# Kernel optimization log

Hardware: AMD Instinct MI355X
Metric: run time of the kernel (lower is better)

Reference implementation:

```python
import jax, jax.numpy as jnp
import numpy as np

GROUPS = 32
HEADS = 8
EPS = 1e-5

def setup_inputs() -> dict:
    key = jax.random.key(0)
    ks = jax.random.split(key, 5)
    C = 512
    x = jax.random.normal(ks[0], (8, C, 32, 32), dtype=jnp.float32)
    gn_w = jnp.ones((C,), dtype=jnp.float32)
    gn_b = jnp.zeros((C,), dtype=jnp.float32)
    qkv_w = jax.random.normal(ks[1], (3 * C, C), dtype=jnp.float32) * 0.02
    qkv_b = jnp.zeros((3 * C,), dtype=jnp.float32)
    proj_w = jax.random.normal(ks[2], (C, C), dtype=jnp.float32) * 0.02
    proj_b = jnp.zeros((C,), dtype=jnp.float32)
    return {"x": x, "gn_w": gn_w, "gn_b": gn_b, "qkv_w": qkv_w,
            "qkv_b": qkv_b, "proj_w": proj_w, "proj_b": proj_b}

def reference(x, gn_w, gn_b, qkv_w, qkv_b, proj_w, proj_b):
    B, C, H, W = x.shape
    d = C // HEADS
    # GroupNorm(32, C)
    xg = x.reshape(B, GROUPS, C // GROUPS, H, W)
    mean = xg.mean(axis=(2, 3, 4), keepdims=True)
    var = xg.var(axis=(2, 3, 4), keepdims=True)
    h = ((xg - mean) * jax.lax.rsqrt(var + EPS)).reshape(B, C, H, W)
    h = h * gn_w[None, :, None, None] + gn_b[None, :, None, None]
    # 1x1 conv QKV == channel matmul
    qkv = jnp.einsum('bchw,oc->bohw', h, qkv_w) + qkv_b[None, :, None, None]
    qkv = qkv.reshape(B, 3, HEADS, d, H * W)
    q, k, v = qkv[:, 0], qkv[:, 1], qkv[:, 2]  # [B, heads, d, HW]
    scale = d ** (-0.5)
    # weight[b,h,q,k] = sum_d q[b,h,d,q] * k[b,h,d,k] * scale
    attn = jax.nn.softmax(jnp.einsum('bhdq,bhdk->bhqk', q, k) * scale, axis=-1)
    # out[b,h,d,q] = sum_k v[b,h,d,k] * attn[b,h,q,k]
    out = jnp.einsum('bhdk,bhqk->bhdq', v, attn).reshape(B, C, H, W)
    out = jnp.einsum('bchw,oc->bohw', out, proj_w) + proj_b[None, :, None, None]
    return out + x
```

## Files before the change

### kernel.cpp

```cpp
#include <hip/hip_runtime.h>
#include <math.h>

#define B_    8
#define C_    512
#define HW_   1024
#define O3_   1536
#define HEADS_ 8
#define D_    64
#define G_    32
#define CPG_  16
#define EPS_  1e-5f
#define M_TOT 8192

#define QSCALE (0.125f * 1.44269504088896f)

typedef __bf16 bf16x8 __attribute__((ext_vector_type(8)));
typedef __bf16 bf16x4 __attribute__((ext_vector_type(4)));
typedef float  f32x4  __attribute__((ext_vector_type(4)));

__device__ __forceinline__ void async_copy16(void* lds, const void* g) {
  __builtin_amdgcn_global_load_lds(
      (const __attribute__((address_space(1))) unsigned int*)g,
      (__attribute__((address_space(3))) unsigned int*)lds, 16, 0, 0);
}

__global__ __launch_bounds__(1024) void k_gn(const float* __restrict__ x,
                                             const float* __restrict__ gw,
                                             const float* __restrict__ gb,
                                             __bf16* __restrict__ h,
                                             const float* __restrict__ qw,
                                             const float* __restrict__ pw,
                                             __bf16* __restrict__ qwb,
                                             __bf16* __restrict__ pwb) {
  __shared__ float red[34];
  __shared__ __bf16 T[16 * 1032];
  int tid = threadIdx.x;
  if (blockIdx.x >= B_ * G_) {
    int i0 = (blockIdx.x - B_ * G_) * 1024 + tid;
    for (int i = i0; i < O3_ * C_ / 4; i += 64 * 1024) {
      float4 v = ((const float4*)qw)[i];
      bf16x4 o = {(__bf16)v.x, (__bf16)v.y, (__bf16)v.z, (__bf16)v.w};
      ((bf16x4*)qwb)[i] = o;
    }
    for (int i = i0; i < C_ * C_ / 4; i += 64 * 1024) {
      float4 v = ((const float4*)pw)[i];
      bf16x4 o = {(__bf16)v.x, (__bf16)v.y, (__bf16)v.z, (__bf16)v.w};
      ((bf16x4*)pwb)[i] = o;
    }
    return;
  }
  int bg = blockIdx.x;
  int b = bg >> 5, g = bg & 31;
  const float4* xg4 = (const float4*)(x + ((size_t)(b * C_) + g * CPG_) * HW_);

  float s = 0.f, ss = 0.f;
  for (int i = tid; i < CPG_ * HW_ / 4; i += 1024) {
    float4 v = xg4[i];
    s += v.x + v.y + v.z + v.w;
    ss += v.x * v.x + v.y * v.y + v.z * v.z + v.w * v.w;
  }
  for (int off = 32; off > 0; off >>= 1) {
    s  += __shfl_down(s, off, 64);
    ss += __shfl_down(ss, off, 64);
  }
  int wv = tid >> 6;
  if ((tid & 63) == 0) { red[wv] = s; red[16 + wv] = ss; }
  __syncthreads();
  if (tid == 0) {
    float S = 0.f, SS = 0.f;
#pragma unroll
    for (int i = 0; i < 16; i++) { S += red[i]; SS += red[16 + i]; }
    float mean = S / (float)(CPG_ * HW_);
    float var  = SS / (float)(CPG_ * HW_) - mean * mean;
    red[32] = mean;
    red[33] = rsqrtf(var + EPS_);
  }
  __syncthreads();
  float mean = red[32], rstd = red[33];

  for (int i = tid; i < CPG_ * HW_ / 4; i += 1024) {
    int c = i >> 8;
    int hw4 = (i & 255) * 4;
    float ga = gw[g * CPG_ + c], be = gb[g * CPG_ + c];
    float4 v = xg4[i];
    bf16x4 pk;
    pk[0] = (__bf16)((v.x - mean) * rstd * ga + be);
    pk[1] = (__bf16)((v.y - mean) * rstd * ga + be);
    pk[2] = (__bf16)((v.z - mean) * rstd * ga + be);
    pk[3] = (__bf16)((v.w - mean) * rstd * ga + be);
    *(bf16x4*)(&T[c * 1032 + hw4]) = pk;
  }
  __syncthreads();

  __bf16* hb = h + (size_t)b * HW_ * C_ + g * CPG_;
  for (int j = tid; j < 2 * HW_; j += 1024) {
    int hw = j >> 1, c8 = (j & 1) * 8;
    bf16x8 v;
#pragma unroll
    for (int jj = 0; jj < 8; jj++) v[jj] = T[(c8 + jj) * 1032 + hw];
    *(bf16x8*)(hb + (size_t)hw * C_ + c8) = v;
  }
}

#define BKQ 32
__global__ __launch_bounds__(256, 3) void k_qkv(const __bf16* __restrict__ h,
                                                const __bf16* __restrict__ w,
                                                const float* __restrict__ bias,
                                                __bf16* __restrict__ y,
                                                __bf16* __restrict__ vT) {
  __shared__ __align__(16) __bf16 As[2][128 * BKQ];
  __shared__ __align__(16) __bf16 Bs[2][128 * BKQ];
  int m0 = blockIdx.x * 128, n0 = blockIdx.y * 128;
  int t = threadIdx.x;
  int lane = t & 63, l16 = lane & 15, quad = lane >> 4;
  int wv = t >> 6;
  int wm = (wv >> 1) * 64, wn = (wv & 1) * 64;

  int rsub = lane >> 2;
  int chunk = (lane & 3) ^ (rsub & 3);
  const __bf16* ag = h + (size_t)(m0 + wv * 32 + rsub) * C_ + chunk * 8;
  const __bf16* bg = w + (size_t)(n0 + wv * 32 + rsub) * C_ + chunk * 8;
  int sw = l16 & 3;

  auto stage = [&](int k0, int bi) {
    __bf16* la = As[bi] + wv * 1024 + lane * 8;
    __bf16* lb = Bs[bi] + wv * 1024 + lane * 8;
#pragma unroll
    for (int s = 0; s < 2; s++) {
      async_copy16(la + s * 512, ag + (size_t)(s * 16) * C_ + k0);
      async_copy16(lb + s * 512, bg + (size_t)(s * 16) * C_ + k0);
    }
  };

  f32x4 acc[4][4];
#pragma unroll
  for (int i = 0; i < 4; i++)
#pragma unroll
    for (int j = 0; j < 4; j++) acc[i][j] = f32x4{0.f, 0.f, 0.f, 0.f};

  stage(0, 0);
  stage(1 * BKQ, 1);
  for (int kk = 0; kk < 16; kk++) {
    int bi = kk & 1;
    if (kk < 15)
      asm volatile("s_waitcnt vmcnt(4)\n\ts_barrier" ::: "memory");
    else
      asm volatile("s_waitcnt vmcnt(0)\n\ts_barrier" ::: "memory");
    const __bf16* as = As[bi];
    const __bf16* bs = Bs[bi];
    bf16x8 af[4], bf[4];
#pragma unroll
    for (int i = 0; i < 4; i++) {
      af[i] = *(const bf16x8*)(as + (wm + i * 16 + l16) * BKQ + (quad ^ sw) * 8);
      bf[i] = *(const bf16x8*)(bs + (wn + i * 16 + l16) * BKQ + (quad ^ sw) * 8);
    }
    asm volatile("s_waitcnt lgkmcnt(0)\n\ts_barrier" ::: "memory");
    if (kk < 14) stage((kk + 2) * BKQ, bi);
    __builtin_amdgcn_s_setprio(1);
#pragma unroll
    for (int i = 0; i < 4; i++)
#pragma unroll
      for (int j = 0; j < 4; j++)
        acc[i][j] = __builtin_amdgcn_mfma_f32_16x16x32_bf16(af[i], bf[j],
                                                            acc[i][j], 0, 0, 0);
    __builtin_amdgcn_s_setprio(0);
  }

  if (n0 >= 2 * C_) {
    int bb = m0 >> 10;
    int tokBase = (m0 & 1023) + wm + quad * 4;
#pragma unroll
    for (int j = 0; j < 4; j++) {
      int n = n0 + wn + j * 16 + l16;
      int c = n - 2 * C_;
      float bv = bias[n];
      __bf16* vrow = vT + ((size_t)(bb * C_) + c) * HW_;
#pragma unroll
      for (int i = 0; i < 4; i++) {
        bf16x4 pk;
#pragma unroll
        for (int r = 0; r < 4; r++) pk[r] = (__bf16)(acc[i][j][r] + bv);
        *(bf16x4*)(vrow + tokBase + i * 16) = pk;
      }
    }
  } else {
    float sc = (n0 < C_) ? QSCALE : 1.0f;
#pragma unroll
    for (int j = 0; j < 4; j++) {
      int n = n0 + wn + j * 16 + l16;
      float bv = bias[n];
#pragma unroll
      for (int i = 0; i < 4; i++)
#pragma unroll
        for (int r = 0; r < 4; r++) {
          int m = m0 + wm + i * 16 + quad * 4 + r;
          y[(size_t)m * O3_ + n] = (__bf16)((acc[i][j][r] + bv) * sc);
        }
    }
  }
}

__global__ __launch_bounds__(256, 4) void k_attn(const __bf16* __restrict__ y,
                                                 const __bf16* __restrict__ vT,
                                                 __bf16* __restrict__ ao) {
  __shared__ __align__(16) __bf16 Ks[2][64 * 64];
  __shared__ __align__(16) __bf16 Vt[2][64 * 64];
  __shared__ __align__(16) __bf16 Pp[4][16 * 36];
  int hd = blockIdx.x, b = blockIdx.y, qt = blockIdx.z;
  int t = threadIdx.x;
  int wv = t >> 6, lane = t & 63, l16 = lane & 15, quad = lane >> 4;
  int q0 = qt * 64 + wv * 16;

  const __bf16* base = y + (size_t)(b * HW_) * O3_ + hd * D_;
  const __bf16* kg = base + C_;
  const __bf16* vtg = vT + ((size_t)(b * C_) + hd * D_) * HW_;

  bf16x8 qb[2];
#pragma unroll
  for (int dh = 0; dh < 2; dh++)
    qb[dh] = *(const bf16x8*)(base + (size_t)(q0 + l16) * O3_ +
                              dh * 32 + quad * 8);

  int rowsub = lane >> 3;
  int kChunk = (lane & 7) ^ (rowsub & 7);

  auto stage = [&](int kt, int bi) {
#pragma unroll
    for (int s = 0; s < 2; s++) {
      int row = wv * 16 + s * 8 + rowsub;
      async_copy16(&Ks[bi][(wv * 16 + s * 8) * 64 + lane * 8],
                   kg + (size_t)(kt + row) * O3_ + kChunk * 8);
    }
#pragma unroll
    for (int s = 0; s < 2; s++) {
      int row = wv * 16 + s * 8 + rowsub;
      async_copy16(&Vt[bi][(wv * 16 + s * 8) * 64 + lane * 8],
                   vtg + (size_t)row * HW_ + kt + kChunk * 8);
    }
  };

  float l_run = 0.f;
  f32x4 o_acc[4];
#pragma unroll
  for (int dt = 0; dt < 4; dt++) o_acc[dt] = f32x4{0.f, 0.f, 0.f, 0.f};

  f32x4 sE[2], sO[2];

  auto QK = [&](f32x4 (&st)[2], const __bf16* ks, int kh) {
    __builtin_amdgcn_s_setprio(1);
#pragma unroll
    for (int tti = 0; tti < 2; tti++) {
      int row = kh * 32 + tti * 16 + l16;
      bf16x8 ka0 = *(const bf16x8*)(&ks[row * 64 + ((quad) ^ (l16 & 7)) * 8]);
      bf16x8 ka1 = *(const bf16x8*)(&ks[row * 64 + ((4 + quad) ^ (l16 & 7)) * 8]);
      f32x4 z = {0.f, 0.f, 0.f, 0.f};
      st[tti] = __builtin_amdgcn_mfma_f32_16x16x32_bf16(ka0, qb[0], z, 0, 0, 0);
      st[tti] = __builtin_amdgcn_mfma_f32_16x16x32_bf16(ka1, qb[1], st[tti], 0, 0, 0);
    }
    __builtin_amdgcn_s_setprio(0);
  };

  auto FIN = [&](f32x4 (&st)[2], const __bf16* vs, int kh) {
    float rs = 0.f;
#pragma unroll
    for (int tti = 0; tti < 2; tti++)
#pragma unroll
      for (int r = 0; r < 4; r++) {
        float e = __builtin_amdgcn_exp2f(st[tti][r]);
        st[tti][r] = e;
        rs += e;
      }
    l_run += rs;
#pragma unroll
    for (int tti = 0; tti < 2; tti++) {
      bf16x4 pk;
#pragma unroll
      for (int r = 0; r < 4; r++) pk[r] = (__bf16)st[tti][r];
      *(bf16x4*)(&Pp[wv][l16 * 36 + tti * 16 + quad * 4]) = pk;
    }
    asm volatile("s_waitcnt lgkmcnt(0)" ::: "memory");
    bf16x8 pb = *(const bf16x8*)(&Pp[wv][l16 * 36 + quad * 8]);
    __builtin_amdgcn_s_setprio(1);
#pragma unroll
    for (int dt = 0; dt < 4; dt++) {
      bf16x8 va = *(const bf16x8*)(&vs[(dt * 16 + l16) * 64 +
                                       ((kh * 4 + quad) ^ (l16 & 7)) * 8]);
      o_acc[dt] = __builtin_amdgcn_mfma_f32_16x16x32_bf16(va, pb,
                                                          o_acc[dt], 0, 0, 0);
    }
    __builtin_amdgcn_s_setprio(0);
  };

  stage(0, 0);

  for (int step = 0; step < 16; step++) {
    int bi = step & 1;
    asm volatile("s_waitcnt vmcnt(0)\n\ts_barrier" ::: "memory");
    if (step < 15) stage((step + 1) * 64, bi ^ 1);

    const __bf16* ks = Ks[bi];
    const __bf16* vs = Vt[bi];
    QK(sE, ks, 0);
    QK(sO, ks, 1); FIN(sE, vs, 0);
    FIN(sO, vs, 1);
  }

  l_run += __shfl_xor(l_run, 16, 64);
  l_run += __shfl_xor(l_run, 32, 64);
  float inv = 1.f / l_run;

#pragma unroll
  for (int dt = 0; dt < 4; dt++) {
    bf16x4 pk;
#pragma unroll
    for (int r = 0; r < 4; r++) pk[r] = (__bf16)(o_acc[dt][r] * inv);
    int ch = hd * D_ + dt * 16 + quad * 4;
    *(bf16x4*)(ao + (size_t)(b * HW_ + q0 + l16) * C_ + ch) = pk;
  }
}

#define BK 64
__global__ __launch_bounds__(256) void k_proj(const __bf16* __restrict__ ao,
                                              const __bf16* __restrict__ w,
                                              const float* __restrict__ bias,
                                              const float* __restrict__ x,
                                              float* __restrict__ out) {
  __shared__ __align__(16) __bf16 As[2][128 * BK];
  __shared__ __align__(16) __bf16 Bs[2][64 * BK];
  int n0 = blockIdx.x * 64, m0 = blockIdx.y * 128;
  int t = threadIdx.x;
  int lane = t & 63, l16 = lane & 15, quad = lane >> 4;
  int wv = t >> 6;
  int wm = (wv >> 1) * 64, wn = (wv & 1) * 32;

  int rsub = lane >> 3;
  int chunk = (lane & 7) ^ rsub;
  const __bf16* ag = w + (size_t)(m0 + wv * 32 + rsub) * C_ + chunk * 8;
  const __bf16* bg = ao + (size_t)(n0 + wv * 16 + rsub) * C_ + chunk * 8;
  int sw = l16 & 7;

  auto stage = [&](int k0, int bi) {
    __bf16* la = As[bi] + wv * 2048 + lane * 8;
    __bf16* lb = Bs[bi] + wv * 1024 + lane * 8;
#pragma unroll
    for (int s = 0; s < 4; s++)
      async_copy16(la + s * 512, ag + (size_t)(s * 8) * C_ + k0);
#pragma unroll
    for (int s = 0; s < 2; s++)
      async_copy16(lb + s * 512, bg + (size_t)(s * 8) * C_ + k0);
  };

  f32x4 acc[4][2];
#pragma unroll
  for (int i = 0; i < 4; i++)
#pragma unroll
    for (int j = 0; j < 2; j++) acc[i][j] = f32x4{0.f, 0.f, 0.f, 0.f};

  stage(0, 0);
  stage(1 * BK, 1);
  for (int kk = 0; kk < 8; kk++) {
    int bi = kk & 1;
    if (kk < 7)
      asm volatile("s_waitcnt vmcnt(6)\n\ts_barrier" ::: "memory");
    else
      asm volatile("s_waitcnt vmcnt(0)\n\ts_barrier" ::: "memory");
    const __bf16* as = As[bi];
    const __bf16* bs = Bs[bi];
    bf16x8 af[2][4], bf[2][2];
#pragma unroll
    for (int hh = 0; hh < 2; hh++) {
#pragma unroll
      for (int i = 0; i < 4; i++)
        af[hh][i] = *(const bf16x8*)(as + (wm + i * 16 + l16) * BK +
                                     ((hh * 4 + quad) ^ sw) * 8);
#pragma unroll
      for (int j = 0; j < 2; j++)
        bf[hh][j] = *(const bf16x8*)(bs + (wn + j * 16 + l16) * BK +
                                     ((hh * 4 + quad) ^ sw) * 8);
    }
    asm volatile("s_waitcnt lgkmcnt(0)\n\ts_barrier" ::: "memory");
    if (kk < 6) stage((kk + 2) * BK, bi);
    __builtin_amdgcn_s_setprio(1);
#pragma unroll
    for (int hh = 0; hh < 2; hh++)
#pragma unroll
      for (int i = 0; i < 4; i++)
#pragma unroll
        for (int j = 0; j < 2; j++)
          acc[i][j] = __builtin_amdgcn_mfma_f32_16x16x32_bf16(af[hh][i], bf[hh][j],
                                                              acc[i][j], 0, 0, 0);
    __builtin_amdgcn_s_setprio(0);
  }

  int bb = n0 >> 10;
#pragma unroll
  for (int i = 0; i < 4; i++)
#pragma unroll
    for (int r = 0; r < 4; r++) {
      int o = m0 + wm + i * 16 + quad * 4 + r;
      float bv = bias[o];
#pragma unroll
      for (int j = 0; j < 2; j++) {
        int n = n0 + wn + j * 16 + l16;
        int hw = n & 1023;
        size_t idx = ((size_t)(bb * C_ + o)) * HW_ + hw;
        out[idx] = acc[i][j][r] + bv + x[idx];
      }
    }
}

extern "C" void kernel_launch(void* const* d_in, const int* in_sizes, int n_in,
                              void* d_out, int out_size, void* d_ws, size_t ws_size,
                              hipStream_t stream) {
  const float* x      = (const float*)d_in[0];
  const float* gn_w   = (const float*)d_in[1];
  const float* gn_b   = (const float*)d_in[2];
  const float* qkv_w  = (const float*)d_in[3];
  const float* qkv_b  = (const float*)d_in[4];
  const float* proj_w = (const float*)d_in[5];
  const float* proj_b = (const float*)d_in[6];
  float* out = (float*)d_out;

  char* ws = (char*)d_ws;
  __bf16* h   = (__bf16*)(ws);
  __bf16* qwb = (__bf16*)(ws + 8388608);
  __bf16* pwb = (__bf16*)(ws + 8388608 + 1572864);
  __bf16* yq  = (__bf16*)(ws + 8388608 + 1572864 + 524288);
  __bf16* ao  = (__bf16*)(ws + 8388608 + 1572864 + 524288 + 25165824);
  __bf16* vT  = (__bf16*)(ws + 8388608 + 1572864 + 524288 + 25165824 + 8388608);

  k_gn  <<<B_ * G_ + 64, 1024, 0, stream>>>(x, gn_w, gn_b, h,
                                            qkv_w, proj_w, qwb, pwb);
  k_qkv <<<dim3(M_TOT / 128, O3_ / 128, 1), 256, 0, stream>>>(h, qwb, qkv_b, yq, vT);
  k_attn<<<dim3(HEADS_, B_, 16), 256, 0, stream>>>(yq, vT, ao);
  k_proj<<<dim3(M_TOT / 64, C_ / 128, 1), 256, 0, stream>>>(ao, pwb, proj_b, x, out);
  (void)in_sizes; (void)n_in; (void)out_size; (void)ws_size;
}
```

Baseline: 142.7 us.

## Load V fragments directly from global into registers and double K tile size

The attention kernel no longer stages V through LDS. Each wave prefetches its V MFMA operands straight from global memory into registers one sub-tile ahead, while the K tile per step grows to 128 keys, halving the barrier count. The QKV GEMM changes its LDS swizzle and swaps MFMA operand order for Q/K outputs, so each lane holds four consecutive columns and can write packed bf16x4 stores with vector bias loads instead of scalar stores. The risk is more register pressure and uncoalesced, redundant global V reads across waves, since every wave loads the full V slice itself.

```diff
diff --git a/kernel.cpp b/kernel.cpp
--- a/kernel.cpp
+++ b/kernel.cpp
@@ -115,12 +115,13 @@
   int lane = t & 63, l16 = lane & 15, quad = lane >> 4;
   int wv = t >> 6;
   int wm = (wv >> 1) * 64, wn = (wv & 1) * 64;
+  bool vreg = (n0 >= 2 * C_);
 
   int rsub = lane >> 2;
-  int chunk = (lane & 3) ^ (rsub & 3);
+  int chunk = (lane & 3) ^ ((rsub >> 1) & 3);
   const __bf16* ag = h + (size_t)(m0 + wv * 32 + rsub) * C_ + chunk * 8;
   const __bf16* bg = w + (size_t)(n0 + wv * 32 + rsub) * C_ + chunk * 8;
-  int sw = l16 & 3;
+  int sw = (l16 >> 1) & 3;
 
   auto stage = [&](int k0, int bi) {
     __bf16* la = As[bi] + wv * 1024 + lane * 8;
@@ -157,16 +158,25 @@
     asm volatile("s_waitcnt lgkmcnt(0)\n\ts_barrier" ::: "memory");
     if (kk < 14) stage((kk + 2) * BKQ, bi);
     __builtin_amdgcn_s_setprio(1);
-#pragma unroll
-    for (int i = 0; i < 4; i++)
-#pragma unroll
-      for (int j = 0; j < 4; j++)
-        acc[i][j] = __builtin_amdgcn_mfma_f32_16x16x32_bf16(af[i], bf[j],
-                                                            acc[i][j], 0, 0, 0);
+    if (vreg) {
+#pragma unroll
+      for (int i = 0; i < 4; i++)
+#pragma unroll
+        for (int j = 0; j < 4; j++)
+          acc[i][j] = __builtin_amdgcn_mfma_f32_16x16x32_bf16(af[i], bf[j],
+                                                              acc[i][j], 0, 0, 0);
+    } else {
+#pragma unroll
+      for (int i = 0; i < 4; i++)
+#pragma unroll
+        for (int j = 0; j < 4; j++)
+          acc[i][j] = __builtin_amdgcn_mfma_f32_16x16x32_bf16(bf[j], af[i],
+                                                              acc[i][j], 0, 0, 0);
+    }
     __builtin_amdgcn_s_setprio(0);
   }
 
-  if (n0 >= 2 * C_) {
+  if (vreg) {
     int bb = m0 >> 10;
     int tokBase = (m0 & 1023) + wm + quad * 4;
 #pragma unroll
@@ -187,15 +197,18 @@
     float sc = (n0 < C_) ? QSCALE : 1.0f;
 #pragma unroll
     for (int j = 0; j < 4; j++) {
-      int n = n0 + wn + j * 16 + l16;
-      float bv = bias[n];
-#pragma unroll
-      for (int i = 0; i < 4; i++)
-#pragma unroll
-        for (int r = 0; r < 4; r++) {
-          int m = m0 + wm + i * 16 + quad * 4 + r;
-          y[(size_t)m * O3_ + n] = (__bf16)((acc[i][j][r] + bv) * sc);
-        }
+      int nb = n0 + wn + j * 16 + quad * 4;
+      float4 bv4 = *(const float4*)(bias + nb);
+      float bvs[4] = {bv4.x, bv4.y, bv4.z, bv4.w};
+#pragma unroll
+      for (int i = 0; i < 4; i++) {
+        int m = m0 + wm + i * 16 + l16;
+        bf16x4 pk;
+#pragma unroll
+        for (int r = 0; r < 4; r++)
+          pk[r] = (__bf16)((acc[i][j][r] + bvs[r]) * sc);
+        *(bf16x4*)(y + (size_t)m * O3_ + nb) = pk;
+      }
     }
   }
 }
@@ -203,8 +216,7 @@
 __global__ __launch_bounds__(256, 4) void k_attn(const __bf16* __restrict__ y,
                                                  const __bf16* __restrict__ vT,
                                                  __bf16* __restrict__ ao) {
-  __shared__ __align__(16) __bf16 Ks[2][64 * 64];
-  __shared__ __align__(16) __bf16 Vt[2][64 * 64];
+  __shared__ __align__(16) __bf16 Ks[2][128 * 64];
   __shared__ __align__(16) __bf16 Pp[4][16 * 36];
   int hd = blockIdx.x, b = blockIdx.y, qt = blockIdx.z;
   int t = threadIdx.x;
@@ -214,6 +226,7 @@
   const __bf16* base = y + (size_t)(b * HW_) * O3_ + hd * D_;
   const __bf16* kg = base + C_;
   const __bf16* vtg = vT + ((size_t)(b * C_) + hd * D_) * HW_;
+  const __bf16* vfb = vtg + (size_t)l16 * HW_ + quad * 8;
 
   bf16x8 qb[2];
 #pragma unroll
@@ -221,21 +234,15 @@
     qb[dh] = *(const bf16x8*)(base + (size_t)(q0 + l16) * O3_ +
                               dh * 32 + quad * 8);
 
-  int rowsub = lane >> 3;
-  int kChunk = (lane & 7) ^ (rowsub & 7);
+  int kRowSub = lane >> 3;
+  int kChunk = (lane & 7) ^ (kRowSub & 7);
 
   auto stage = [&](int kt, int bi) {
 #pragma unroll
-    for (int s = 0; s < 2; s++) {
-      int row = wv * 16 + s * 8 + rowsub;
-      async_copy16(&Ks[bi][(wv * 16 + s * 8) * 64 + lane * 8],
+    for (int s = 0; s < 4; s++) {
+      int row = wv * 32 + s * 8 + kRowSub;
+      async_copy16(&Ks[bi][(wv * 32 + s * 8) * 64 + lane * 8],
                    kg + (size_t)(kt + row) * O3_ + kChunk * 8);
-    }
-#pragma unroll
-    for (int s = 0; s < 2; s++) {
-      int row = wv * 16 + s * 8 + rowsub;
-      async_copy16(&Vt[bi][(wv * 16 + s * 8) * 64 + lane * 8],
-                   vtg + (size_t)row * HW_ + kt + kChunk * 8);
     }
   };
 
@@ -245,12 +252,19 @@
   for (int dt = 0; dt < 4; dt++) o_acc[dt] = f32x4{0.f, 0.f, 0.f, 0.f};
 
   f32x4 sE[2], sO[2];
+  bf16x8 vaE[4], vaO[4];
+
+  auto PFV = [&](bf16x8 (&va)[4], int off) {
+#pragma unroll
+    for (int dt = 0; dt < 4; dt++)
+      va[dt] = *(const bf16x8*)(vfb + (size_t)(dt * 16) * HW_ + off);
+  };
 
   auto QK = [&](f32x4 (&st)[2], const __bf16* ks, int kh) {
     __builtin_amdgcn_s_setprio(1);
 #pragma unroll
     for (int tti = 0; tti < 2; tti++) {
-      int row = kh * 32 + tti * 16 + l16;
+      int row = (kh * 2 + tti) * 16 + l16;
       bf16x8 ka0 = *(const bf16x8*)(&ks[row * 64 + ((quad) ^ (l16 & 7)) * 8]);
       bf16x8 ka1 = *(const bf16x8*)(&ks[row * 64 + ((4 + quad) ^ (l16 & 7)) * 8]);
       f32x4 z = {0.f, 0.f, 0.f, 0.f};
@@ -260,7 +274,7 @@
     __builtin_amdgcn_s_setprio(0);
   };
 
-  auto FIN = [&](f32x4 (&st)[2], const __bf16* vs, int kh) {
+  auto FIN = [&](f32x4 (&st)[2], bf16x8 (&va)[4]) {
     float rs = 0.f;
 #pragma unroll
     for (int tti = 0; tti < 2; tti++)
@@ -282,27 +296,27 @@
     bf16x8 pb = *(const bf16x8*)(&Pp[wv][l16 * 36 + quad * 8]);
     __builtin_amdgcn_s_setprio(1);
 #pragma unroll
-    for (int dt = 0; dt < 4; dt++) {
-      bf16x8 va = *(const bf16x8*)(&vs[(dt * 16 + l16) * 64 +
-                                       ((kh * 4 + quad) ^ (l16 & 7)) * 8]);
-      o_acc[dt] = __builtin_amdgcn_mfma_f32_16x16x32_bf16(va, pb,
+    for (int dt = 0; dt < 4; dt++)
+      o_acc[dt] = __builtin_amdgcn_mfma_f32_16x16x32_bf16(va[dt], pb,
                                                           o_acc[dt], 0, 0, 0);
-    }
     __builtin_amdgcn_s_setprio(0);
   };
 
   stage(0, 0);
-
-  for (int step = 0; step < 16; step++) {
+  PFV(vaE, 0);
+
+  for (int step = 0; step < 8; step++) {
     int bi = step & 1;
     asm volatile("s_waitcnt vmcnt(0)\n\ts_barrier" ::: "memory");
-    if (step < 15) stage((step + 1) * 64, bi ^ 1);
-
+    if (step < 7) stage((step + 1) * 128, bi ^ 1);
+    int kt = step * 128;
+    int ktn = (step < 7) ? (step + 1) * 128 : kt;
     const __bf16* ks = Ks[bi];
-    const __bf16* vs = Vt[bi];
-    QK(sE, ks, 0);
-    QK(sO, ks, 1); FIN(sE, vs, 0);
-    FIN(sO, vs, 1);
+    QK(sE, ks, 0); PFV(vaO, kt + 32);
+    QK(sO, ks, 1); FIN(sE, vaE); PFV(vaE, kt + 64);
+    QK(sE, ks, 2); FIN(sO, vaO); PFV(vaO, kt + 96);
+    QK(sO, ks, 3); FIN(sE, vaE); PFV(vaE, ktn);
+    FIN(sO, vaO);
   }
 
   l_run += __shfl_xor(l_run, 16, 64);
```

Result: slower. 188.5 us (+32.1%).
